# Performance work log

Hardware: AMD Instinct MI355X
Metric: run time of the kernel (lower is better)

The kernel has to match this reference:

```python
import jax, jax.numpy as jnp
import numpy as np

N = 4_000_000      # batch of scalar angles (x[i].item() loop in the torch code)
DEPTH = 10         # qsp_depth -> 2*DEPTH+1 = 21 phase params


def setup_inputs() -> dict:
    key = jax.random.key(0)
    k1, k2, k3 = jax.random.split(key, 3)
    x = jax.random.normal(k1, (N,), dtype=jnp.float32)
    qsp_params = jax.random.uniform(k2, (2 * DEPTH + 1,), dtype=jnp.float32,
                                    minval=0.0, maxval=2.0 * np.pi)
    alphas = jax.random.uniform(k3, (N,), dtype=jnp.float32, minval=0.5, maxval=1.5)
    return {"x": x, "qsp_params": qsp_params, "alphas": alphas}


def _qsp_expectation(x, qsp_params):
    """Standard QSP: U = S(phi_0) prod_{k=1..2d} [W(theta) S(phi_k)], return Re(U[0,0]).
    W(theta) = [[cos t, i sin t], [i sin t, cos t]],  S(phi) = diag(e^{i phi}, e^{-i phi}).
    Vectorized over the batch; lax.scan over the 2*depth phase steps."""
    cc = x.astype(jnp.complex64)
    c = jnp.cos(cc)
    isn = 1j * jnp.sin(cc)
    # signal operator per sample, constant across depth steps: [N, 2, 2]
    W = jnp.stack([jnp.stack([c, isn], -1), jnp.stack([isn, c], -1)], -2)
    ph = jnp.exp(1j * qsp_params.astype(jnp.complex64))  # [2d+1]
    d0 = jnp.stack([ph[0], jnp.conj(ph[0])])             # diag of S(phi_0)
    M0 = jnp.broadcast_to(jnp.eye(2, dtype=jnp.complex64) * d0, W.shape)  # [N,2,2]

    def step(M, p):
        d = jnp.stack([p, jnp.conj(p)])                  # diag of S(phi_k)
        M = jnp.einsum('nij,njk->nik', M, W) * d         # M @ W @ S(phi_k)
        return M, None

    M, _ = jax.lax.scan(step, M0, ph[1:])
    return jnp.real(M[:, 0, 0]).astype(jnp.float32)      # Re(<0|U|0>)


def reference(x, qsp_params, alphas):
    # matches torch: preds[i] = alphas[i] * expectation_value(qsp_params, x[i]); unsqueeze(1)
    return (alphas * _qsp_expectation(x, qsp_params))[:, None]
```

## Files before the change

kernel.cpp:

```cpp
#include <hip/hip_runtime.h>

#define NPARAMS 21
#define INV_2PI 0.15915494309189535f
#define INV_PI  0.3183098861837907f

typedef float v4f __attribute__((ext_vector_type(4)));

__device__ __forceinline__ float sin_rev(float rev) {
    return __builtin_amdgcn_sinf(__builtin_amdgcn_fractf(rev));
}
__device__ __forceinline__ float cos_rev(float rev) {
    return __builtin_amdgcn_cosf(__builtin_amdgcn_fractf(rev));
}

__global__ void coeff_kernel(const float* __restrict__ qsp, float* __restrict__ ws)
{
    __shared__ float g[NPARAMS];
    const int t = threadIdx.x;

    if (t < NPARAMS) {
        const float rev_x = (float)t * (1.0f / 42.0f);
        const float c = cos_rev(rev_x);
        const float s = sin_rev(rev_x);

        float pr = qsp[0] * INV_2PI;
        float ar = cos_rev(pr), ai = sin_rev(pr);
        float br = 0.0f, bi = 0.0f;

        for (int k = 1; k < NPARAMS; ++k) {
            const float pk = qsp[k] * INV_2PI;
            const float cp = cos_rev(pk);
            const float sp = sin_rev(pk);
            const float t1r = c * ar - s * bi;
            const float t1i = c * ai + s * br;
            const float t2r = c * br - s * ai;
            const float t2i = c * bi + s * ar;
            ar = cp * t1r - sp * t1i;
            ai = cp * t1i + sp * t1r;
            br = cp * t2r + sp * t2i;
            bi = cp * t2i - sp * t2r;
        }
        g[t] = ar;
    }
    __syncthreads();

    if (t < 24) {
        float coef = 0.0f;
        if (t == 0) {
            float acc = 0.0f;
            for (int i = 0; i < NPARAMS; ++i) acc += g[i];
            coef = acc * (1.0f / 21.0f);
        } else if (t <= 10) {
            float acc = 0.0f;
            for (int i = 0; i < NPARAMS; ++i)
                acc += g[i] * cos_rev((float)(t * i) * (1.0f / 21.0f));
            coef = acc * (2.0f / 21.0f);
        } else if (t <= 20) {
            const int j = t - 10;
            float acc = 0.0f;
            for (int i = 0; i < NPARAMS; ++i)
                acc += g[i] * sin_rev((float)(j * i) * (1.0f / 21.0f));
            coef = acc * (2.0f / 21.0f);
        }
        ws[t] = coef;
    }
}

__global__ __launch_bounds__(256) void eval_kernel(
    const float* __restrict__ x,
    const float* __restrict__ alphas,
    const float* __restrict__ coefs,
    float* __restrict__ out,
    int n)
{
    const int base = (blockIdx.x * blockDim.x + threadIdx.x) * 8;
    if (base >= n) return;

    const v4f* c4 = reinterpret_cast<const v4f*>(coefs);
    const v4f k0 = c4[0];
    const v4f k1 = c4[1];
    const v4f k2 = c4[2];
    const v4f k3 = c4[3];
    const v4f k4 = c4[4];
    const v4f k5 = c4[5];
    const float P0 = k0.x, P1 = k0.y, P2 = k0.z, P3 = k0.w;
    const float P4 = k1.x, P5 = k1.y, P6 = k1.z, P7 = k1.w;
    const float P8 = k2.x, P9 = k2.y, P10 = k2.z;
    const float Q1 = k2.w, Q2 = k3.x, Q3 = k3.y, Q4 = k3.z, Q5 = k3.w;
    const float Q6 = k4.x, Q7 = k4.y, Q8 = k4.z, Q9 = k4.w, Q10 = k5.x;

    auto eval1 = [&](float xv) -> float {
        const float f  = __builtin_amdgcn_fractf(xv * INV_PI);
        const float s1 = __builtin_amdgcn_sinf(f);
        const float c1 = __builtin_amdgcn_cosf(f);
        const float tc = c1 + c1;
        const float c2  = fmaf(tc, c1, -1.0f);
        const float s2  = tc * s1;
        const float c3  = fmaf(tc, c2, -c1);
        const float s3  = fmaf(tc, s2, -s1);
        const float c4_ = fmaf(tc, c3, -c2);
        const float s4_ = fmaf(tc, s3, -s2);
        const float c5  = fmaf(tc, c4_, -c3);
        const float s5  = fmaf(tc, s4_, -s3);
        const float c6  = fmaf(tc, c5, -c4_);
        const float s6  = fmaf(tc, s5, -s4_);
        const float c7  = fmaf(tc, c6, -c5);
        const float s7  = fmaf(tc, s6, -s5);
        const float c8  = fmaf(tc, c7, -c6);
        const float s8  = fmaf(tc, s7, -s6);
        const float c9  = fmaf(tc, c8, -c7);
        const float s9  = fmaf(tc, s8, -s7);
        const float c10 = fmaf(tc, c9, -c8);
        const float s10 = fmaf(tc, s9, -s8);
        float aP = fmaf(P1, c1, P0);
        float aQ = Q1 * s1;
        aP = fmaf(P2, c2, aP);   aQ = fmaf(Q2, s2, aQ);
        aP = fmaf(P3, c3, aP);   aQ = fmaf(Q3, s3, aQ);
        aP = fmaf(P4, c4_, aP);  aQ = fmaf(Q4, s4_, aQ);
        aP = fmaf(P5, c5, aP);   aQ = fmaf(Q5, s5, aQ);
        aP = fmaf(P6, c6, aP);   aQ = fmaf(Q6, s6, aQ);
        aP = fmaf(P7, c7, aP);   aQ = fmaf(Q7, s7, aQ);
        aP = fmaf(P8, c8, aP);   aQ = fmaf(Q8, s8, aQ);
        aP = fmaf(P9, c9, aP);   aQ = fmaf(Q9, s9, aQ);
        aP = fmaf(P10, c10, aP); aQ = fmaf(Q10, s10, aQ);
        return aP + aQ;
    };

    const v4f* xp = reinterpret_cast<const v4f*>(x + base);
    const v4f* ap = reinterpret_cast<const v4f*>(alphas + base);
    const v4f xa = xp[0], xb = xp[1];
    const v4f aa = ap[0], ab = ap[1];

    v4f oa, ob;
    oa.x = aa.x * eval1(xa.x);
    oa.y = aa.y * eval1(xa.y);
    oa.z = aa.z * eval1(xa.z);
    oa.w = aa.w * eval1(xa.w);
    ob.x = ab.x * eval1(xb.x);
    ob.y = ab.y * eval1(xb.y);
    ob.z = ab.z * eval1(xb.z);
    ob.w = ab.w * eval1(xb.w);

    v4f* op = reinterpret_cast<v4f*>(out + base);
    __builtin_nontemporal_store(oa, op);
    __builtin_nontemporal_store(ob, op + 1);
}

extern "C" void kernel_launch(void* const* d_in, const int* in_sizes, int n_in,
                              void* d_out, int out_size, void* d_ws, size_t ws_size,
                              hipStream_t stream)
{
    const float* x      = (const float*)d_in[0];
    const float* qsp    = (const float*)d_in[1];
    const float* alphas = (const float*)d_in[2];
    float* out          = (float*)d_out;
    float* wsf          = (float*)d_ws;

    const int n = in_sizes[0];

    coeff_kernel<<<1, 64, 0, stream>>>(qsp, wsf);

    const int threads  = 256;
    const int nthreads = (n + 7) / 8;
    const int blocks   = (nthreads + threads - 1) / threads;
    eval_kernel<<<blocks, threads, 0, stream>>>(x, alphas, wsf, out, n);
}
```

Measured before the change: 83.36 us.

## Fuse coefficient computation into eval kernel, recomputing per block

Each block now computes the Chebyshev/Fourier coefficients of the QSP polynomial into shared memory, then evaluates its samples. This drops the separate single-block coefficient kernel launch and its workspace round trip. In exchange every block does redundant trig work and two barriers before it issues its global loads.

Result: no change. 82.80 us (-0.7%).

```diff
diff --git a/kernel.cpp b/kernel.cpp
--- a/kernel.cpp
+++ b/kernel.cpp
@@ -13,9 +13,15 @@
     return __builtin_amdgcn_cosf(__builtin_amdgcn_fractf(rev));
 }
 
-__global__ void coeff_kernel(const float* __restrict__ qsp, float* __restrict__ ws)
+__global__ __launch_bounds__(256) void qsp_fused_kernel(
+    const float* __restrict__ x,
+    const float* __restrict__ qsp,
+    const float* __restrict__ alphas,
+    float* __restrict__ out,
+    int n)
 {
     __shared__ float g[NPARAMS];
+    __shared__ float coef[NPARAMS];
     const int t = threadIdx.x;
 
     if (t < NPARAMS) {
@@ -44,50 +50,34 @@
     }
     __syncthreads();
 
-    if (t < 24) {
-        float coef = 0.0f;
+    if (t < NPARAMS) {
+        float acc = 0.0f;
         if (t == 0) {
-            float acc = 0.0f;
             for (int i = 0; i < NPARAMS; ++i) acc += g[i];
-            coef = acc * (1.0f / 21.0f);
+            acc *= (1.0f / 21.0f);
         } else if (t <= 10) {
-            float acc = 0.0f;
             for (int i = 0; i < NPARAMS; ++i)
                 acc += g[i] * cos_rev((float)(t * i) * (1.0f / 21.0f));
-            coef = acc * (2.0f / 21.0f);
-        } else if (t <= 20) {
+            acc *= (2.0f / 21.0f);
+        } else {
             const int j = t - 10;
-            float acc = 0.0f;
             for (int i = 0; i < NPARAMS; ++i)
                 acc += g[i] * sin_rev((float)(j * i) * (1.0f / 21.0f));
-            coef = acc * (2.0f / 21.0f);
+            acc *= (2.0f / 21.0f);
         }
-        ws[t] = coef;
+        coef[t] = acc;
     }
-}
+    __syncthreads();
 
-__global__ __launch_bounds__(256) void eval_kernel(
-    const float* __restrict__ x,
-    const float* __restrict__ alphas,
-    const float* __restrict__ coefs,
-    float* __restrict__ out,
-    int n)
-{
-    const int base = (blockIdx.x * blockDim.x + threadIdx.x) * 8;
+    const float P0 = coef[0],  P1 = coef[1],  P2 = coef[2],  P3 = coef[3];
+    const float P4 = coef[4],  P5 = coef[5],  P6 = coef[6],  P7 = coef[7];
+    const float P8 = coef[8],  P9 = coef[9],  P10 = coef[10];
+    const float Q1 = coef[11], Q2 = coef[12], Q3 = coef[13], Q4 = coef[14];
+    const float Q5 = coef[15], Q6 = coef[16], Q7 = coef[17], Q8 = coef[18];
+    const float Q9 = coef[19], Q10 = coef[20];
+
+    const int base = (blockIdx.x * blockDim.x + t) * 8;
     if (base >= n) return;
-
-    const v4f* c4 = reinterpret_cast<const v4f*>(coefs);
-    const v4f k0 = c4[0];
-    const v4f k1 = c4[1];
-    const v4f k2 = c4[2];
-    const v4f k3 = c4[3];
-    const v4f k4 = c4[4];
-    const v4f k5 = c4[5];
-    const float P0 = k0.x, P1 = k0.y, P2 = k0.z, P3 = k0.w;
-    const float P4 = k1.x, P5 = k1.y, P6 = k1.z, P7 = k1.w;
-    const float P8 = k2.x, P9 = k2.y, P10 = k2.z;
-    const float Q1 = k2.w, Q2 = k3.x, Q3 = k3.y, Q4 = k3.z, Q5 = k3.w;
-    const float Q6 = k4.x, Q7 = k4.y, Q8 = k4.z, Q9 = k4.w, Q10 = k5.x;
 
     auto eval1 = [&](float xv) -> float {
         const float f  = __builtin_amdgcn_fractf(xv * INV_PI);
@@ -154,14 +144,11 @@
     const float* qsp    = (const float*)d_in[1];
     const float* alphas = (const float*)d_in[2];
     float* out          = (float*)d_out;
-    float* wsf          = (float*)d_ws;
 
     const int n = in_sizes[0];
-
-    coeff_kernel<<<1, 64, 0, stream>>>(qsp, wsf);
 
     const int threads  = 256;
     const int nthreads = (n + 7) / 8;
     const int blocks   = (nthreads + threads - 1) / threads;
-    eval_kernel<<<blocks, threads, 0, stream>>>(x, alphas, wsf, out, n);
+    qsp_fused_kernel<<<blocks, threads, 0, stream>>>(x, qsp, alphas, out, n);
 }
```
